# Kernel tuning notes

Hardware: AMD Instinct MI355X
Metric: run time of the kernel (lower is better)

## Reference

```python
import jax, jax.numpy as jnp
import numpy as np

L, B, D, H, DH, M = 1024, 2, 1024, 16, 64, 1024
T = L + M
SCALE = 1.0 / np.sqrt(DH).astype(np.float32)
NEG = -1e30


def _rel_shift(x):
    # x: [L, T, B, H] -- Transformer-XL relative shift along axis 1
    qlen, klen = x.shape[0], x.shape[1]
    zero_pad = jnp.zeros((qlen, 1) + x.shape[2:], x.dtype)
    x_padded = jnp.concatenate([zero_pad, x], axis=1)          # [L, T+1, B, H]
    x_padded = x_padded.reshape((klen + 1, qlen) + x.shape[2:])
    return x_padded[1:].reshape(x.shape)


def setup_inputs() -> dict:
    key = jax.random.key(0)
    ks = jax.random.split(key, 9)
    init = lambda k, shp, s: jax.random.normal(k, shp, jnp.float32) * s
    x = init(ks[0], (L, B, D), 1.0)
    memory = init(ks[1], (M, B, D), 1.0)
    pos_emb = init(ks[2], (T, B, D), 1.0)
    pos_bias_u = init(ks[3], (H, DH), 0.02)
    pos_bias_v = init(ks[4], (H, DH), 0.02)
    s = 1.0 / np.sqrt(D)
    Wq = init(ks[5], (D, H * DH), s)
    Wkv = init(ks[6], (D, 2 * H * DH), s)
    Wrel = init(ks[7], (D, H * DH), s)
    Wo = init(ks[8], (H * DH, D), 1.0 / np.sqrt(H * DH))
    gamma = jnp.ones((D,), jnp.float32)
    beta = jnp.zeros((D,), jnp.float32)
    # causal mask: key position j valid iff j <= i + mem_len
    i = jnp.arange(L)[:, None]
    j = jnp.arange(T)[None, :]
    mask = jnp.broadcast_to((j > i + M)[:, :, None], (L, T, B))
    return dict(x=x, pos_emb=pos_emb, memory=memory, pos_bias_u=pos_bias_u,
                pos_bias_v=pos_bias_v, mask=mask, Wq=Wq, Wkv=Wkv, Wrel=Wrel,
                Wo=Wo, gamma=gamma, beta=beta)


def reference(x, pos_emb, memory, pos_bias_u, pos_bias_v, mask, Wq, Wkv, Wrel, Wo, gamma, beta):
    # vanilla path: memory has same batch size as x
    c = jnp.concatenate([memory, x], axis=0)                   # [T, B, D]
    k, v = jnp.split(c @ Wkv, 2, axis=-1)                      # [T, B, H*DH] each
    q = (x @ Wq).reshape(L, B, H, DH)
    k = k.reshape(T, B, H, DH)
    v = v.reshape(T, B, H, DH)
    r = (pos_emb @ Wrel).reshape(T, B, H, DH)
    AC = jnp.einsum('ibnd,jbnd->ijbn', q + pos_bias_u, k)      # content term
    BD = jnp.einsum('ibnd,jbnd->ijbn', q + pos_bias_v, r)      # position term
    BD = _rel_shift(BD)
    attn_score = (AC + BD) * SCALE                             # [L, T, B, H]
    attn_score = jnp.where(mask[:, :, :, None], NEG, attn_score)
    attn_prob = jax.nn.softmax(attn_score, axis=1)
    attn_matrix = attn_prob.mean(axis=(2, 3))                  # [L, T]
    attn_vec = jnp.einsum('ijbn,jbnd->ibnd', attn_prob, v).reshape(L, B, H * DH)
    attn_out = attn_vec @ Wo                                   # [L, B, D]
    h = x + attn_out
    mu = h.mean(-1, keepdims=True)
    var = h.var(-1, keepdims=True)
    output = (h - mu) / jnp.sqrt(var + 1e-5) * gamma + beta
    return output, attn_matrix
```

## Files before the change

### kernel.cpp

```cpp
#include <hip/hip_runtime.h>
#include <math.h>
#include <stdint.h>

#define L_  1024
#define B_  2
#define D_  1024
#define H_  16
#define DH_ 64
#define M_  1024
#define T_  2048
#define SCALE_ 0.125f
#define SCALE2_ 0.18033688f

typedef unsigned short ushort;
typedef short bf16x8 __attribute__((ext_vector_type(8)));
typedef float f32x4 __attribute__((ext_vector_type(4)));
typedef unsigned short u16x4v __attribute__((ext_vector_type(4)));
typedef unsigned short u16x8v __attribute__((ext_vector_type(8)));

#define MFMA16(a,b,c) __builtin_amdgcn_mfma_f32_16x16x32_bf16(a,b,c,0,0,0)

#if __has_builtin(__builtin_amdgcn_exp2f)
#define EXP2(x) __builtin_amdgcn_exp2f(x)
#else
#define EXP2(x) exp2f(x)
#endif

static __device__ __forceinline__ ushort f2bf(float x) {
    uint32_t u = __float_as_uint(x);
    uint32_t r = (u + 0x7FFFu + ((u >> 16) & 1u)) >> 16;
    return (ushort)r;
}
static __device__ __forceinline__ ushort f2bf_fast(float x) {
    return (ushort)((__float_as_uint(x) + 0x8000u) >> 16);
}
static __device__ __forceinline__ float bf2f(ushort h) {
    return __uint_as_float(((uint32_t)h) << 16);
}
static __device__ __forceinline__ void gl_lds16(const ushort* g, ushort* l) {
    __builtin_amdgcn_global_load_lds(
        (const __attribute__((address_space(1))) void*)g,
        (__attribute__((address_space(3))) void*)l, 16, 0, 0);
}

static __device__ const unsigned char GRP_OF[85] = {
 0,0,0,0, 1,1,1,1, 2,2,2,2, 3,3,3,3,
 4,4,4,4,4, 5,5,5,5,5, 6,6,6,6,6, 7,7,7,7,7, 8,8,8,8,8,
 9,9,9,9,9,9, 10,10,10,10,10,10, 11,11,11,11,11,11,
 12,12,12,12,12,12, 13,13,13,13,13,13,
 14,14,14,14,14,14,14, 15,15,15,15,15,15,15};
static __device__ const unsigned char SLC_OF[85] = {
 0,1,2,3, 0,1,2,3, 0,1,2,3, 0,1,2,3,
 0,1,2,3,4, 0,1,2,3,4, 0,1,2,3,4, 0,1,2,3,4, 0,1,2,3,4,
 0,1,2,3,4,5, 0,1,2,3,4,5, 0,1,2,3,4,5,
 0,1,2,3,4,5, 0,1,2,3,4,5,
 0,1,2,3,4,5,6, 0,1,2,3,4,5,6};
static __device__ const unsigned char NS_OF[16] = {4,4,4,4,5,5,5,5,5,6,6,6,6,6,7,7};

__global__ __launch_bounds__(256) void prep(
    const float* __restrict__ memory, const float* __restrict__ x,
    const float* __restrict__ pos_emb,
    const float* __restrict__ Wq, const float* __restrict__ Wkv,
    const float* __restrict__ Wrel, const float* __restrict__ Wo,
    ushort* __restrict__ cb, ushort* __restrict__ pb,
    ushort* __restrict__ Wqt, ushort* __restrict__ Wkvt,
    ushort* __restrict__ Wrelt, ushort* __restrict__ Wot,
    float* __restrict__ lpart)
{
    __shared__ float t[32][33];
    int tid = threadIdx.x;
    if (blockIdx.x >= 9216) {
        int i = ((blockIdx.x - 9216) * 256 + tid) * 4;
        *(float4*)(lpart + i) = (float4){0.f, 0.f, 0.f, 0.f};
        return;
    }
    if (blockIdx.x < 4096) {
        int idx = (blockIdx.x * 256 + tid) * 8;
        const float* s;
        ushort* d;
        if (idx < 2097152)      { s = memory + idx;              d = cb + idx; }
        else if (idx < 4194304) { s = x + (idx - 2097152);       d = cb + idx; }
        else                    { s = pos_emb + (idx - 4194304); d = pb + (idx - 4194304); }
        float4 a = *(const float4*)(s);
        float4 b = *(const float4*)(s + 4);
        u16x8v o;
        o[0] = f2bf(a.x); o[1] = f2bf(a.y); o[2] = f2bf(a.z); o[3] = f2bf(a.w);
        o[4] = f2bf(b.x); o[5] = f2bf(b.y); o[6] = f2bf(b.z); o[7] = f2bf(b.w);
        *(u16x8v*)d = o;
        return;
    }
    int tb = blockIdx.x - 4096;
    const float* src; ushort* dst; int N;
    if (tb < 1024)      { src = Wq;   dst = Wqt;   N = 1024; }
    else if (tb < 3072) { src = Wkv;  dst = Wkvt;  N = 2048; tb -= 1024; }
    else if (tb < 4096) { src = Wrel; dst = Wrelt; N = 1024; tb -= 3072; }
    else                { src = Wo;   dst = Wot;   N = 1024; tb -= 4096; }
    int k0 = (tb & 31) * 32, n0 = (tb >> 5) * 32;
    int r = tid >> 3, c4 = (tid & 7) * 4;
    float4 v = *(const float4*)(src + (size_t)(k0 + r) * N + n0 + c4);
    t[r][c4 + 0] = v.x; t[r][c4 + 1] = v.y; t[r][c4 + 2] = v.z; t[r][c4 + 3] = v.w;
    __syncthreads();
    u16x4v o;
    o[0] = f2bf(t[c4 + 0][r]); o[1] = f2bf(t[c4 + 1][r]);
    o[2] = f2bf(t[c4 + 2][r]); o[3] = f2bf(t[c4 + 3][r]);
    *(u16x4v*)(dst + (size_t)(n0 + r) * 1024 + k0 + c4) = o;
}

__global__ __launch_bounds__(256) void proj_all(
    const ushort* __restrict__ cb, const ushort* __restrict__ pb,
    const ushort* __restrict__ Wqt, const ushort* __restrict__ Wkvt,
    const ushort* __restrict__ Wrelt,
    const float* __restrict__ bu, const float* __restrict__ bv,
    ushort* __restrict__ quB, ushort* __restrict__ qvB,
    ushort* __restrict__ kbB, ushort* __restrict__ VtB,
    ushort* __restrict__ rbB)
{
    __shared__ ushort Al[128 * 32];
    __shared__ ushort Bl[128 * 32];
    int lin = blockIdx.x;
    int omode, M0, N0;
    const ushort *A, *Wt;
    if (lin < 128) {
        omode = 0; A = cb + 2097152; Wt = Wqt;
        M0 = (lin & 15) * 128; N0 = (lin >> 4) * 128;
    } else if (lin < 640) {
        omode = 1; A = cb; Wt = Wkvt;
        int l2 = lin - 128;
        M0 = (l2 & 31) * 128; N0 = (l2 >> 5) * 128;
    } else {
        omode = 2; A = pb; Wt = Wrelt;
        int l2 = lin - 640;
        M0 = (l2 & 31) * 128; N0 = (l2 >> 5) * 128;
    }
    int tid = threadIdx.x;
    int wid = tid >> 6, lane = tid & 63, quad = lane >> 4, jl = lane & 15;
    int wr = wid >> 1, wc = wid & 1;
    int srow = lane >> 2;
    int scol = (lane & 3) * 8;

    f32x4 acc[4][4];
    #pragma unroll
    for (int i = 0; i < 4; ++i)
        #pragma unroll
        for (int j = 0; j < 4; ++j) acc[i][j] = (f32x4){0.f, 0.f, 0.f, 0.f};

    for (int k0 = 0; k0 < 1024; k0 += 32) {
        #pragma unroll
        for (int c = 0; c < 2; ++c) {
            int r = wid * 32 + c * 16 + srow;
            gl_lds16(A  + (size_t)(M0 + r) * 1024 + k0 + scol,
                     Al + wid * 1024 + c * 512);
            gl_lds16(Wt + (size_t)(N0 + r) * 1024 + k0 + scol,
                     Bl + wid * 1024 + c * 512);
        }
        __syncthreads();
        bf16x8 af[4], bfr[4];
        #pragma unroll
        for (int mt = 0; mt < 4; ++mt)
            af[mt] = *(const bf16x8*)&Al[(wr * 64 + mt * 16 + jl) * 32 + quad * 8];
        #pragma unroll
        for (int nt = 0; nt < 4; ++nt)
            bfr[nt] = *(const bf16x8*)&Bl[(wc * 64 + nt * 16 + jl) * 32 + quad * 8];
        #pragma unroll
        for (int mt = 0; mt < 4; ++mt)
            #pragma unroll
            for (int nt = 0; nt < 4; ++nt)
                acc[mt][nt] = MFMA16(af[mt], bfr[nt], acc[mt][nt]);
        __syncthreads();
    }

    #pragma unroll
    for (int mt = 0; mt < 4; ++mt)
        #pragma unroll
        for (int nt = 0; nt < 4; ++nt)
            #pragma unroll
            for (int r = 0; r < 4; ++r) {
                int gm = M0 + wr * 64 + mt * 16 + quad * 4 + r;
                int gn = N0 + wc * 64 + nt * 16 + jl;
                float v = acc[mt][nt][r];
                if (omode == 0) {
                    int l = gm >> 1, b = gm & 1;
                    int h = gn >> 6, d = gn & 63;
                    size_t o = ((size_t)((b << 4) | h) * 1024 + l) * 64 + d;
                    quB[o] = f2bf(v + bu[gn]);
                    qvB[o] = f2bf(v + bv[gn]);
                } else if (omode == 1) {
                    int t = gm >> 1, b = gm & 1;
                    int nn = gn & 1023;
                    int h = nn >> 6, d = nn & 63;
                    if (gn < 1024)
                        kbB[((size_t)((b << 4) | h) * 2048 + t) * 64 + d] = f2bf(v);
                    else {
                        int tp = (t & ~63) | ((t & 15) << 2) | ((t >> 4) & 3);
                        VtB[((size_t)((b << 4) | h) * 64 + d) * 2048 + tp] = f2bf(v);
                    }
                } else {
                    int t = gm >> 1, b = gm & 1;
                    int h = gn >> 6, d = gn & 63;
                    rbB[((size_t)((b << 4) | h) * 2048 + t) * 64 + d] = f2bf(v);
                }
            }
}

__global__ __launch_bounds__(256) void attn_score(
    const ushort* __restrict__ qu, const ushort* __restrict__ qv,
    const ushort* __restrict__ kb, const ushort* __restrict__ rb,
    float* __restrict__ lpart, ushort* __restrict__ AMw)
{
    __shared__ ushort Kl[2][64 * 64];
    __shared__ ushort Rl[2][128 * 64];

    int tid = threadIdx.x, wid = tid >> 6, lane = tid & 63;
    int quad = lane >> 4, jl = lane & 15, jx = jl & 7;

    int lin  = blockIdx.x;
    int xcd  = lin & 7;
    int rest = lin >> 3;
    int bh   = (xcd << 2) | (rest & 3);
    int sidx = rest >> 2;
    int grp  = GRP_OF[sidx];
    int slc  = SLC_OF[sidx];
    int nc   = 17 + grp;
    int ns   = NS_OF[grp];
    int cb_  = slc * nc / ns;
    int ce_  = (slc + 1) * nc / ns;
    int it   = grp * 4 + wid;
    int i0w  = it * 16;
    int irow = i0w + quad * 4;

    const ushort* kp  = kb + (size_t)bh * 2048 * 64;
    const ushort* rp  = rb + (size_t)bh * 2048 * 64;
    const ushort* qup = qu + (size_t)bh * 1024 * 64;
    const ushort* qvp = qv + (size_t)bh * 1024 * 64;

    bf16x8 quA[2], qvA[2];
    quA[0] = *(const bf16x8*)(qup + (size_t)(i0w + jl) * 64 + quad * 8);
    quA[1] = *(const bf16x8*)(qup + (size_t)(i0w + jl) * 64 + 32 + quad * 8);
    qvA[0] = *(const bf16x8*)(qvp + (size_t)(i0w + jl) * 64 + quad * 8);
    qvA[1] = *(const bf16x8*)(qvp + (size_t)(i0w + jl) * 64 + 32 + quad * 8);

    ushort* prow0 = AMw + ((size_t)irow * 32 + bh) * 2048 + jl * 4;

    int lrow = lane >> 3;
    int scol = ((lane & 7) ^ lrow) * 8;

    f32x4 z = (f32x4){0.f, 0.f, 0.f, 0.f};
    float lsum[4] = {0.f, 0.f, 0.f, 0.f};

    auto stage = [&](int b_, int c) {
        int j0n = c * 64;
        int rbase = 960 + j0n - grp * 64;
        ushort* KB = &Kl[b_][0];
        ushort* RB = &Rl[b_][0];
        #pragma unroll
        for (int q = 0; q < 6; ++q) {
            int rgn = wid * 6 + q;
            if (rgn < 8) {
                int row = rgn * 8 + lrow;
                gl_lds16(kp + (size_t)(j0n + row) * 64 + scol, KB + rgn * 512);
            } else {
                int row = (rgn - 8) * 8 + lrow;
                int rg = rbase + row;
                rg = rg > 2047 ? 2047 : rg;
                gl_lds16(rp + (size_t)rg * 64 + scol, RB + (rgn - 8) * 512);
            }
        }
        __builtin_amdgcn_sched_barrier(0);
    };

    int buf = 0;
    stage(0, cb_);
    asm volatile("s_waitcnt vmcnt(0)" ::: "memory");
    __builtin_amdgcn_sched_barrier(0);
    __builtin_amdgcn_s_barrier();

    for (int c = cb_; c < ce_; ++c) {
        if (c + 1 < ce_) stage(buf ^ 1, c + 1);
        int j0 = c * 64;
        int d0 = 1008 + j0 - i0w;
        bool interior = (j0 + 63 <= i0w + M_) && (d0 + 79 <= 2047);
        const ushort* KB = &Kl[buf][0];
        const ushort* RB = &Rl[buf][0];
        f32x4 ac[4];
        #pragma unroll
        for (int su = 0; su < 4; ++su) {
            int row = su * 16 + jl;
            int s0 = (quad ^ jx) * 8;
            bf16x8 k0v = *(const bf16x8*)&KB[row * 64 + s0];
            bf16x8 k1v = *(const bf16x8*)&KB[row * 64 + (s0 ^ 32)];
            f32x4 t = MFMA16(quA[0], k0v, z);
            ac[su] = MFMA16(quA[1], k1v, t);
        }
        int ob = 48 - wid * 16 + jl;
        f32x4 bt[5];
        #pragma unroll
        for (int nt = 0; nt < 5; ++nt) {
            int o = ob + nt * 16;
            int s0 = (quad ^ jx) * 8;
            bf16x8 r0 = *(const bf16x8*)&RB[o * 64 + s0];
            bf16x8 r1 = *(const bf16x8*)&RB[o * 64 + (s0 ^ 32)];
            f32x4 t = MFMA16(qvA[0], r0, z);
            bt[nt] = MFMA16(qvA[1], r1, t);
        }
        float bs[4][5];
        #pragma unroll
        for (int r = 0; r < 4; ++r) {
            int ii = quad * 4 + r;
            int src = (quad << 4) | ((jl + 15 - ii) & 15);
            #pragma unroll
            for (int nt = 0; nt < 5; ++nt) bs[r][nt] = __shfl(bt[nt][r], src);
        }
        if (interior) {
            #pragma unroll
            for (int r = 0; r < 4; ++r) {
                int ii = quad * 4 + r;
                bool hi = (jl > ii);
                u16x4v ps;
                #pragma unroll
                for (int su = 0; su < 4; ++su) {
                    float bd = hi ? bs[r][su + 1] : bs[r][su];
                    float p = EXP2(fminf((ac[su][r] + bd) * SCALE2_, 86.f));
                    lsum[r] += p;
                    ps[su] = f2bf_fast(p);
                }
                *(u16x4v*)(prow0 + (size_t)r * 65536 + j0) = ps;
            }
        } else {
            #pragma unroll
            for (int r = 0; r < 4; ++r) {
                int ii = quad * 4 + r;
                bool hi = (jl > ii);
                u16x4v ps;
                #pragma unroll
                for (int su = 0; su < 4; ++su) {
                    float bd = hi ? bs[r][su + 1] : bs[r][su];
                    float sv = (ac[su][r] + bd) * SCALE2_;
                    int j = j0 + su * 16 + jl;
                    float p = (j <= irow + r + M_) ? EXP2(fminf(sv, 86.f)) : 0.f;
                    lsum[r] += p;
                    ps[su] = f2bf_fast(p);
                }
                *(u16x4v*)(prow0 + (size_t)r * 65536 + j0) = ps;
            }
        }
        asm volatile("s_waitcnt vmcnt(4)" ::: "memory");
        __builtin_amdgcn_sched_barrier(0);
        __builtin_amdgcn_s_barrier();
        buf ^= 1;
    }

    #pragma unroll
    for (int r = 0; r < 4; ++r) {
        #pragma unroll
        for (int off = 1; off < 16; off <<= 1) lsum[r] += __shfl_xor(lsum[r], off);
        if (jl == 0) atomicAdd(&lpart[(size_t)bh * 1024 + irow + r], lsum[r]);
    }
}

__global__ __launch_bounds__(256) void pv_gemm(
    const ushort* __restrict__ P, const ushort* __restrict__ Vt,
    const float* __restrict__ lpart,
    ushort* __restrict__ OvecB, float* __restrict__ linvs)
{
    __shared__ ushort Al[64][40];
    __shared__ ushort Bl[64][40];
    int tid = threadIdx.x;
    int lin  = blockIdx.x;
    int xcd  = lin & 7;
    int rest = lin >> 3;
    int bh   = (xcd << 2) | (rest & 3);
    int mt   = rest >> 2;
    int M0   = mt * 64;
    int wid = tid >> 6, lane = tid & 63, quad = lane >> 4, jl = lane & 15;
    int m0w = (wid >> 1) * 32, n0w = (wid & 1) * 32;
    int sr = tid >> 2, sc = (tid & 3) * 8;

    const ushort* Bp = Vt + (size_t)bh * 64 * 2048;
    int kend = (17 + mt) * 64;

    f32x4 acc[2][2];
    #pragma unroll
    for (int i = 0; i < 2; ++i)
        #pragma unroll
        for (int j = 0; j < 2; ++j) acc[i][j] = (f32x4){0.f, 0.f, 0.f, 0.f};

    for (int k0 = 0; k0 < kend; k0 += 32) {
        *(u16x8v*)&Al[sr][sc] =
            *(const u16x8v*)(P + ((size_t)(M0 + sr) * 32 + bh) * 2048 + k0 + sc);
        *(u16x8v*)&Bl[sr][sc] = *(const u16x8v*)(Bp + (size_t)sr * 2048 + k0 + sc);
        __syncthreads();
        bf16x8 a0 = *(const bf16x8*)&Al[m0w + jl][quad * 8];
        bf16x8 a1 = *(const bf16x8*)&Al[m0w + 16 + jl][quad * 8];
        bf16x8 b0 = *(const bf16x8*)&Bl[n0w + jl][quad * 8];
        bf16x8 b1 = *(const bf16x8*)&Bl[n0w + 16 + jl][quad * 8];
        acc[0][0] = MFMA16(a0, b0, acc[0][0]);
        acc[0][1] = MFMA16(a0, b1, acc[0][1]);
        acc[1][0] = MFMA16(a1, b0, acc[1][0]);
        acc[1][1] = MFMA16(a1, b1, acc[1][1]);
        __syncthreads();
    }

    int b = bh >> 4, h = bh & 15;
    #pragma unroll
    for (int ms = 0; ms < 2; ++ms)
        #pragma unroll
        for (int r = 0; r < 4; ++r) {
            int gi = M0 + m0w + 16 * ms + quad * 4 + r;
            float linv = 1.f / lpart[(size_t)bh * 1024 + gi];
            #pragma unroll
            for (int ns = 0; ns < 2; ++ns) {
                int gd = n0w + 16 * ns + jl;
                OvecB[(size_t)(gi * 2 + b) * 1024 + h * 64 + gd] =
                    f2bf(acc[ms][ns][r] * linv);
            }
            if (n0w == 0 && jl == 0)
                linvs[(size_t)gi * 32 + bh] = linv * 0.03125f;
        }
}

__global__ __launch_bounds__(256) void tail_fused(
    const ushort* __restrict__ A, const ushort* __restrict__ Wt,
    const float* __restrict__ resid, float* __restrict__ outF,
    const ushort* __restrict__ AMw, const float* __restrict__ linvs,
    float* __restrict__ AM)
{
    __shared__ ushort Al[64][40];
    __shared__ ushort Bl[64][40];
    int tid = threadIdx.x;
    int lin = blockIdx.x;
    if (lin >= 512) {
        __shared__ float lv[32];
        __shared__ float jbuf[2048];
        int i = lin - 512;
        if (tid < 32) lv[tid] = linvs[(size_t)i * 32 + tid];
        __syncthreads();
        int k0 = tid * 8;
        int jmax = i + M_;
        float acc[8];
        #pragma unroll
        for (int e = 0; e < 8; ++e) acc[e] = 0.f;
        if ((k0 & ~63) <= jmax) {
            const ushort* base = AMw + (size_t)i * 65536;
            for (int p = 0; p < 32; ++p) {
                float l = lv[p];
                u16x8v v = *(const u16x8v*)(base + (size_t)p * 2048 + k0);
                #pragma unroll
                for (int e = 0; e < 8; ++e) acc[e] += bf2f(v[e]) * l;
            }
        }
        #pragma unroll
        for (int e = 0; e < 8; ++e) {
            int kp = k0 + e;
            int j  = (kp & ~63) | ((kp & 3) << 4) | ((kp >> 2) & 15);
            jbuf[j] = acc[e];
        }
        __syncthreads();
        int j0 = tid * 8;
        float4 o0, o1;
        o0.x = (j0 + 0 <= jmax) ? jbuf[j0 + 0] : 0.f;
        o0.y = (j0 + 1 <= jmax) ? jbuf[j0 + 1] : 0.f;
        o0.z = (j0 + 2 <= jmax) ? jbuf[j0 + 2] : 0.f;
        o0.w = (j0 + 3 <= jmax) ? jbuf[j0 + 3] : 0.f;
        o1.x = (j0 + 4 <= jmax) ? jbuf[j0 + 4] : 0.f;
        o1.y = (j0 + 5 <= jmax) ? jbuf[j0 + 5] : 0.f;
        o1.z = (j0 + 6 <= jmax) ? jbuf[j0 + 6] : 0.f;
        o1.w = (j0 + 7 <= jmax) ? jbuf[j0 + 7] : 0.f;
        *(float4*)(AM + (size_t)i * 2048 + j0) = o0;
        *(float4*)(AM + (size_t)i * 2048 + j0 + 4) = o1;
        return;
    }
    int M0 = (lin & 31) * 64, N0 = (lin >> 5) * 64;
    int wid = tid >> 6, lane = tid & 63, quad = lane >> 4, jl = lane & 15;
    int m0w = (wid >> 1) * 32, n0w = (wid & 1) * 32;
    int sr = tid >> 2, sc = (tid & 3) * 8;

    f32x4 acc[2][2];
    #pragma unroll
    for (int i = 0; i < 2; ++i)
        #pragma unroll
        for (int j = 0; j < 2; ++j) acc[i][j] = (f32x4){0.f, 0.f, 0.f, 0.f};

    for (int k0 = 0; k0 < 1024; k0 += 32) {
        *(u16x8v*)&Al[sr][sc] = *(const u16x8v*)(A  + (size_t)(M0 + sr) * 1024 + k0 + sc);
        *(u16x8v*)&Bl[sr][sc] = *(const u16x8v*)(Wt + (size_t)(N0 + sr) * 1024 + k0 + sc);
        __syncthreads();
        bf16x8 a0 = *(const bf16x8*)&Al[m0w + jl][quad * 8];
        bf16x8 a1 = *(const bf16x8*)&Al[m0w + 16 + jl][quad * 8];
        bf16x8 b0 = *(const bf16x8*)&Bl[n0w + jl][quad * 8];
        bf16x8 b1 = *(const bf16x8*)&Bl[n0w + 16 + jl][quad * 8];
        acc[0][0] = MFMA16(a0, b0, acc[0][0]);
        acc[0][1] = MFMA16(a0, b1, acc[0][1]);
        acc[1][0] = MFMA16(a1, b0, acc[1][0]);
        acc[1][1] = MFMA16(a1, b1, acc[1][1]);
        __syncthreads();
    }

    #pragma unroll
    for (int ms = 0; ms < 2; ++ms)
        #pragma unroll
        for (int ns = 0; ns < 2; ++ns)
            #pragma unroll
            for (int r = 0; r < 4; ++r) {
                int gm = M0 + m0w + 16 * ms + quad * 4 + r;
                int gn = N0 + n0w + 16 * ns + jl;
                outF[(size_t)gm * 1024 + gn] =
                    acc[ms][ns][r] + resid[(size_t)gm * 1024 + gn];
            }
}

__global__ __launch_bounds__(256) void ln_kernel(
    const float* __restrict__ hbuf,
    const float* __restrict__ gamma, const float* __restrict__ beta,
    float* __restrict__ out)
{
    __shared__ float rs[4], rss[4];
    int row = blockIdx.x;
    int tid = threadIdx.x;
    const float* hp = hbuf + (size_t)row * 1024;
    float4 h4 = *(const float4*)(hp + (tid << 2));
    float s = h4.x + h4.y + h4.z + h4.w;
    float ss = h4.x * h4.x + h4.y * h4.y + h4.z * h4.z + h4.w * h4.w;
    #pragma unroll
    for (int o = 32; o > 0; o >>= 1) {
        s  += __shfl_down(s, o);
        ss += __shfl_down(ss, o);
    }
    if ((tid & 63) == 0) { rs[tid >> 6] = s; rss[tid >> 6] = ss; }
    __syncthreads();
    float tot  = rs[0] + rs[1] + rs[2] + rs[3];
    float tots = rss[0] + rss[1] + rss[2] + rss[3];
    float mu = tot * (1.f / 1024.f);
    float var = tots * (1.f / 1024.f) - mu * mu;
    float rstd = rsqrtf(var + 1e-5f);
    float4 g4 = *(const float4*)(gamma + (tid << 2));
    float4 b4 = *(const float4*)(beta + (tid << 2));
    float4 o4;
    o4.x = (h4.x - mu) * rstd * g4.x + b4.x;
    o4.y = (h4.y - mu) * rstd * g4.y + b4.y;
    o4.z = (h4.z - mu) * rstd * g4.z + b4.z;
    o4.w = (h4.w - mu) * rstd * g4.w + b4.w;
    *(float4*)(out + (size_t)row * 1024 + (tid << 2)) = o4;
}

extern "C" void kernel_launch(void* const* d_in, const int* in_sizes, int n_in,
                              void* d_out, int out_size, void* d_ws, size_t ws_size,
                              hipStream_t stream) {
    const float* x       = (const float*)d_in[0];
    const float* pos_emb = (const float*)d_in[1];
    const float* memory  = (const float*)d_in[2];
    const float* bu      = (const float*)d_in[3];
    const float* bv      = (const float*)d_in[4];
    const float* Wq      = (const float*)d_in[6];
    const float* Wkv     = (const float*)d_in[7];
    const float* Wrel    = (const float*)d_in[8];
    const float* Wo      = (const float*)d_in[9];
    const float* gamma   = (const float*)d_in[10];
    const float* beta    = (const float*)d_in[11];

    float* out = (float*)d_out;
    float* AM  = out + (size_t)2097152;

    ushort* cb    = (ushort*)d_ws;
    ushort* pb    = cb    + 4194304;
    ushort* Wqt   = pb    + 4194304;
    ushort* Wkvt  = Wqt   + 1048576;
    ushort* Wrelt = Wkvt  + 2097152;
    ushort* Wot   = Wrelt + 1048576;
    ushort* quB   = Wot   + 1048576;
    ushort* qvB   = quB   + 2097152;
    ushort* kbB   = qvB   + 2097152;
    ushort* VtB   = kbB   + 4194304;
    ushort* rbB   = VtB   + 4194304;
    ushort* OvecB = rbB   + 4194304;
    float*  hbuf  = (float*)(OvecB + 2097152);
    float*  lpart = hbuf  + 2097152;
    float*  linvs = lpart + 32768;
    ushort* AMw   = (ushort*)(linvs + 32768);

    dim3 blk(256);
    prep<<<9248, blk, 0, stream>>>(memory, x, pos_emb, Wq, Wkv, Wrel, Wo,
                                   cb, pb, Wqt, Wkvt, Wrelt, Wot, lpart);
    proj_all<<<896, blk, 0, stream>>>(cb, pb, Wqt, Wkvt, Wrelt, bu, bv,
                                      quB, qvB, kbB, VtB, rbB);
    attn_score<<<dim3(2720), blk, 0, stream>>>(quB, qvB, kbB, rbB, lpart, AMw);
    pv_gemm<<<dim3(512), blk, 0, stream>>>(AMw, VtB, lpart, OvecB, linvs);
    tail_fused<<<dim3(1536), blk, 0, stream>>>(OvecB, Wot, x, hbuf,
                                               AMw, linvs, AM);
    ln_kernel<<<2048, blk, 0, stream>>>(hbuf, gamma, beta, out);
}
```

Before: 293.6 us.

## Double-buffer projection GEMM LDS tiles and swizzle to avoid bank conflicts

The fused QKV/rel projection GEMM now uses two LDS buffers so the next k-slice's global-to-LDS loads are issued before computing on the current slice. This replaces two syncthreads per step with one barrier. It also applies an XOR-style rotation of the 8-element column chunk per row pair, which is meant to reduce LDS bank conflicts on the fragment reads. LDS usage doubles, which may lower occupancy.

```diff
diff --git a/kernel.cpp b/kernel.cpp
--- a/kernel.cpp
+++ b/kernel.cpp
@@ -115,8 +115,8 @@
     ushort* __restrict__ kbB, ushort* __restrict__ VtB,
     ushort* __restrict__ rbB)
 {
-    __shared__ ushort Al[128 * 32];
-    __shared__ ushort Bl[128 * 32];
+    __shared__ ushort Al[2][128 * 32];
+    __shared__ ushort Bl[2][128 * 32];
     int lin = blockIdx.x;
     int omode, M0, N0;
     const ushort *A, *Wt;
@@ -136,7 +136,6 @@
     int wid = tid >> 6, lane = tid & 63, quad = lane >> 4, jl = lane & 15;
     int wr = wid >> 1, wc = wid & 1;
     int srow = lane >> 2;
-    int scol = (lane & 3) * 8;
 
     f32x4 acc[4][4];
     #pragma unroll
@@ -144,29 +143,49 @@
         #pragma unroll
         for (int j = 0; j < 4; ++j) acc[i][j] = (f32x4){0.f, 0.f, 0.f, 0.f};
 
+    auto stage = [&](int b_, int k0) {
+        #pragma unroll
+        for (int c = 0; c < 2; ++c) {
+            int r  = wid * 32 + c * 16 + srow;
+            int su = ((lane & 3) - (r >> 1)) & 3;
+            gl_lds16(A  + (size_t)(M0 + r) * 1024 + k0 + su * 8,
+                     &Al[b_][wid * 1024 + c * 512]);
+            gl_lds16(Wt + (size_t)(N0 + r) * 1024 + k0 + su * 8,
+                     &Bl[b_][wid * 1024 + c * 512]);
+        }
+        __builtin_amdgcn_sched_barrier(0);
+    };
+
+    int buf = 0;
+    stage(0, 0);
+    asm volatile("s_waitcnt vmcnt(0)" ::: "memory");
+    __builtin_amdgcn_sched_barrier(0);
+    __builtin_amdgcn_s_barrier();
+
     for (int k0 = 0; k0 < 1024; k0 += 32) {
-        #pragma unroll
-        for (int c = 0; c < 2; ++c) {
-            int r = wid * 32 + c * 16 + srow;
-            gl_lds16(A  + (size_t)(M0 + r) * 1024 + k0 + scol,
-                     Al + wid * 1024 + c * 512);
-            gl_lds16(Wt + (size_t)(N0 + r) * 1024 + k0 + scol,
-                     Bl + wid * 1024 + c * 512);
-        }
-        __syncthreads();
+        if (k0 + 32 < 1024) stage(buf ^ 1, k0 + 32);
         bf16x8 af[4], bfr[4];
         #pragma unroll
-        for (int mt = 0; mt < 4; ++mt)
-            af[mt] = *(const bf16x8*)&Al[(wr * 64 + mt * 16 + jl) * 32 + quad * 8];
-        #pragma unroll
-        for (int nt = 0; nt < 4; ++nt)
-            bfr[nt] = *(const bf16x8*)&Bl[(wc * 64 + nt * 16 + jl) * 32 + quad * 8];
+        for (int mt = 0; mt < 4; ++mt) {
+            int ra = wr * 64 + mt * 16 + jl;
+            int u  = (quad + (ra >> 1)) & 3;
+            af[mt] = *(const bf16x8*)&Al[buf][ra * 32 + u * 8];
+        }
+        #pragma unroll
+        for (int nt = 0; nt < 4; ++nt) {
+            int rb_ = wc * 64 + nt * 16 + jl;
+            int u   = (quad + (rb_ >> 1)) & 3;
+            bfr[nt] = *(const bf16x8*)&Bl[buf][rb_ * 32 + u * 8];
+        }
         #pragma unroll
         for (int mt = 0; mt < 4; ++mt)
             #pragma unroll
             for (int nt = 0; nt < 4; ++nt)
                 acc[mt][nt] = MFMA16(af[mt], bfr[nt], acc[mt][nt]);
-        __syncthreads();
+        asm volatile("s_waitcnt vmcnt(0)" ::: "memory");
+        __builtin_amdgcn_sched_barrier(0);
+        __builtin_amdgcn_s_barrier();
+        buf ^= 1;
     }
 
     #pragma unroll
```

Measured after the change: 291.3 us. About the same (-0.8%).
